# Performance work log

Measured on AMD Instinct MI355X. Metric: run time of the kernel, lower is better.

Reference implementation:

```python
import jax, jax.numpy as jnp
import numpy as np

K_NEIGHBOURS = 4  # neighbour_num
BN_EPS = 1e-5


def setup_inputs() -> dict:
    key = jax.random.key(0)
    ks = jax.random.split(key, 5)
    B, T, J, C = 32, 243, 17, 256
    std = np.sqrt(2.0 / C).astype(np.float32)
    return {
        "x": jax.random.normal(ks[0], (B, T, J, C), dtype=jnp.float32),
        "W_u": jax.random.normal(ks[1], (C, C), dtype=jnp.float32) * std,
        "b_u": jnp.zeros((C,), dtype=jnp.float32),
        "W_v": jax.random.normal(ks[2], (C, C), dtype=jnp.float32) * std,
        "b_v": jnp.zeros((C,), dtype=jnp.float32),
        "gamma": jnp.ones((T,), dtype=jnp.float32),
        "beta": jnp.zeros((T,), dtype=jnp.float32),
    }


def reference(x, W_u, b_u, W_v, b_v, gamma, beta):
    # temporal-mode GCN with top-k similarity adjacency
    b, t, j, c = x.shape
    xr = jnp.transpose(x, (0, 2, 1, 3)).reshape(b * j, t, c)  # [BJ, T, C]

    # similarity adjacency: keep edges >= k-th largest similarity per row
    sim = jnp.einsum('bnc,bmc->bnm', xr, xr)                  # [BJ, T, T]
    thr = jax.lax.top_k(sim, K_NEIGHBOURS)[0][..., -1:]       # [BJ, T, 1]
    adj = (sim >= thr).astype(x.dtype)

    # symmetric degree normalization D^{-1/2} A D^{-1/2}
    deg_inv_sqrt = adj.sum(-1) ** -0.5                        # [BJ, T]
    norm_adj = deg_inv_sqrt[:, :, None] * adj * deg_inv_sqrt[:, None, :]

    v = xr @ W_v.T + b_v
    u = xr @ W_u.T + b_u
    h = jnp.einsum('bnm,bmc->bnc', norm_adj, v) + u           # [BJ, T, C]

    # BatchNorm1d(num_features=T), training mode: stats over (batch, C)
    mean = h.mean(axis=(0, 2), keepdims=True)
    var = jnp.mean((h - mean) ** 2, axis=(0, 2), keepdims=True)
    hn = (h - mean) * jax.lax.rsqrt(var + BN_EPS) * gamma[None, :, None] + beta[None, :, None]

    out = jax.nn.relu(xr + hn)                                # residual (dim_in == dim_out)
    return jnp.transpose(out.reshape(b, j, t, c), (0, 2, 1, 3))  # [B, T, J, C]
```

## Files before the change

### kernel.cpp

```cpp
#include <hip/hip_runtime.h>

#define BB 32
#define TT 243
#define JJ 17
#define CC 256
#define BJC (BB*JJ)
#define MM (BJC*TT)
#define FR (BJC*256)
#define SIMP 244
#define NEG_INF (-3.0e38f)

typedef __attribute__((ext_vector_type(8))) short bf16x8;
typedef __attribute__((ext_vector_type(4))) float f32x4;
typedef __attribute__((ext_vector_type(8))) _Float16 f16x8;
typedef __attribute__((ext_vector_type(4))) _Float16 f16x4;

__device__ __forceinline__ unsigned short f2bf(float f) {
  unsigned int u = __float_as_uint(f);
  u = (u + 0x7fffu + ((u >> 16) & 1u)) >> 16;
  return (unsigned short)u;
}
__device__ __forceinline__ float bf2f(unsigned short s) {
  return __uint_as_float(((unsigned int)s) << 16);
}

__device__ __forceinline__ void gld16(const void* g, void* l) {
  __builtin_amdgcn_global_load_lds(
      (__attribute__((address_space(1))) void*)(g),
      (__attribute__((address_space(3))) void*)(l), 16, 0, 0);
}

__launch_bounds__(256)
__global__ void k_prep_w(const float* __restrict__ Wu, const float* __restrict__ Wv,
                         _Float16* __restrict__ wcp) {
  const int r = blockIdx.x * 4 + (threadIdx.x >> 6);
  const int l = threadIdx.x & 63;
  const float* src = ((r < CC) ? (Wu + (size_t)r * CC) : (Wv + (size_t)(r - CC) * CC)) + l * 4;
  float4 v = *reinterpret_cast<const float4*>(src);
  f16x4 hv = (f16x4){(_Float16)v.x, (_Float16)v.y, (_Float16)v.z, (_Float16)v.w};
  const int ks = l >> 4;
  const int u  = (l & 15) >> 1;
  const int s  = u ^ (r & 7);
  *reinterpret_cast<f16x4*>(wcp + ((size_t)ks * 512 + r) * 64 + s * 8 + (l & 1) * 4) = hv;
}

__launch_bounds__(256)
__global__ void k_prep_x(const float* __restrict__ x,
                         _Float16* __restrict__ xqh, _Float16* __restrict__ xql) {
  const int r = blockIdx.x * 4 + (threadIdx.x >> 6);
  const int l = threadIdx.x & 63;
  const int bj = r / TT, t = r - bj * TT;
  const int b = bj / JJ, j = bj - b * JJ;
  float4 v = *reinterpret_cast<const float4*>(
      x + ((size_t)(b * TT + t) * JJ + j) * CC + l * 4);
  _Float16 h0 = (_Float16)v.x, h1 = (_Float16)v.y, h2 = (_Float16)v.z, h3 = (_Float16)v.w;
  f16x4 hv = (f16x4){h0, h1, h2, h3};
  f16x4 lv = (f16x4){(_Float16)(v.x - (float)h0), (_Float16)(v.y - (float)h1),
                     (_Float16)(v.z - (float)h2), (_Float16)(v.w - (float)h3)};
  const int fr = bj * 256 + t;
  const int ks = l >> 4;
  const int u  = (l & 15) >> 1;
  const int s  = u ^ (t & 7);
  const size_t off = ((size_t)ks * FR + fr) * 64 + s * 8 + (l & 1) * 4;
  *reinterpret_cast<f16x4*>(xqh + off) = hv;
  *reinterpret_cast<f16x4*>(xql + off) = lv;
}

__launch_bounds__(512)
__global__ void k_sim(const _Float16* __restrict__ xqh, const _Float16* __restrict__ xql,
                      float* __restrict__ sim) {
  __shared__ _Float16 Sh[2][256 * 64];
  __shared__ _Float16 Sl[2][256 * 64];
  const int bj = blockIdx.x;
  const int tid = threadIdx.x, lane = tid & 63, wid = tid >> 6;
  const int wr = wid >> 2, wc = wid & 3;
  const int l15 = lane & 15, lg = lane >> 4;
  const size_t rb = (size_t)bj * 256;
  const size_t lsrc = (size_t)(lane >> 3) * 64 + (lane & 7) * 8;

  f32x4 acc[8][4];
  #pragma unroll
  for (int i = 0; i < 8; i++)
    #pragma unroll
    for (int j = 0; j < 4; j++) acc[i][j] = (f32x4){0.f, 0.f, 0.f, 0.f};

  auto STAGE = [&](int ks, int d) {
    const _Float16* ph = xqh + ((size_t)ks * FR + rb) * 64;
    const _Float16* pl = xql + ((size_t)ks * FR + rb) * 64;
    #pragma unroll
    for (int c = 0; c < 4; ++c) {
      const int row0 = (wid * 4 + c) * 8;
      gld16(ph + (size_t)row0 * 64 + lsrc, &Sh[d][row0 * 64]);
      gld16(pl + (size_t)row0 * 64 + lsrc, &Sl[d][row0 * 64]);
    }
  };
  auto COMPUTE = [&](int d) {
    #pragma unroll
    for (int kh = 0; kh < 2; ++kh) {
      f16x8 bhv[4], blv[4];
      #pragma unroll
      for (int j = 0; j < 4; ++j) {
        int rc = wc * 64 + j * 16 + l15;
        int sl = ((kh * 4 + lg) ^ (rc & 7)) * 8;
        bhv[j] = *reinterpret_cast<const f16x8*>(&Sh[d][rc * 64 + sl]);
        blv[j] = *reinterpret_cast<const f16x8*>(&Sl[d][rc * 64 + sl]);
      }
      #pragma unroll
      for (int i = 0; i < 8; ++i) {
        int rl = wr * 128 + i * 16 + l15;
        int sl = ((kh * 4 + lg) ^ (rl & 7)) * 8;
        f16x8 ah = *reinterpret_cast<const f16x8*>(&Sh[d][rl * 64 + sl]);
        f16x8 al = *reinterpret_cast<const f16x8*>(&Sl[d][rl * 64 + sl]);
        #pragma unroll
        for (int j = 0; j < 4; ++j) {
          acc[i][j] = __builtin_amdgcn_mfma_f32_16x16x32_f16(ah, bhv[j], acc[i][j], 0, 0, 0);
          acc[i][j] = __builtin_amdgcn_mfma_f32_16x16x32_f16(ah, blv[j], acc[i][j], 0, 0, 0);
          acc[i][j] = __builtin_amdgcn_mfma_f32_16x16x32_f16(al, bhv[j], acc[i][j], 0, 0, 0);
        }
      }
    }
  };

  STAGE(0, 0);
  __syncthreads();
  for (int ks = 0; ks < 4; ++ks) {
    if (ks < 3) STAGE(ks + 1, (ks + 1) & 1);
    COMPUTE(ks & 1);
    __syncthreads();
  }

  const size_t sbase = (size_t)bj * TT * SIMP;
  #pragma unroll
  for (int i = 0; i < 8; ++i) {
    #pragma unroll
    for (int q = 0; q < 4; ++q) {
      int n = wr * 128 + i * 16 + lg * 4 + q;
      if (n < TT) {
        #pragma unroll
        for (int j = 0; j < 4; ++j) {
          int c = wc * 64 + j * 16 + l15;
          if (c < TT) sim[sbase + (size_t)n * SIMP + c] = acc[i][j][q];
        }
      }
    }
  }
}

__launch_bounds__(256)
__global__ void k_uv(const _Float16* __restrict__ xqh, const _Float16* __restrict__ wcp,
                     const float* __restrict__ bu, const float* __restrict__ bv,
                     unsigned short* __restrict__ uo, unsigned short* __restrict__ vo) {
  __shared__ _Float16 S[2][128][64];
  const int ct = blockIdx.x;
  const int m0 = blockIdx.y * 128;
  const int tid = threadIdx.x, lane = tid & 63, wid = tid >> 6;
  const int rm = wid * 32;
  const int l15 = lane & 15, lg = lane >> 4;

  const float* bsrc = (ct < 2) ? bu : bv;
  unsigned short* osrc = (ct < 2) ? uo : vo;
  const int cb = (ct & 1) * 128;

  float bias[8];
  #pragma unroll
  for (int j = 0; j < 8; ++j) bias[j] = bsrc[cb + j * 16 + l15];

  f32x4 acc[2][8];
  #pragma unroll
  for (int i = 0; i < 2; i++)
    #pragma unroll
    for (int j = 0; j < 8; j++) acc[i][j] = (f32x4){0.f, 0.f, 0.f, 0.f};

  for (int ks = 0; ks < 4; ++ks) {
    #pragma unroll
    for (int c = 0; c < 8; ++c) {
      int ch = wid * 8 + c;
      int half = ch >> 4;
      int rows0 = (ch & 15) * 8;
      const _Float16* g = half
        ? wcp + ((size_t)ks * 512 + ct * 128 + rows0) * 64 + lane * 8
        : xqh + ((size_t)ks * FR  + m0       + rows0) * 64 + lane * 8;
      gld16(g, &S[half][rows0][0]);
    }
    __syncthreads();
    #pragma unroll
    for (int kh = 0; kh < 2; ++kh) {
      f16x8 af[2], bfv[8];
      #pragma unroll
      for (int i = 0; i < 2; ++i) {
        int rl = rm + i * 16 + l15;
        af[i] = *reinterpret_cast<const f16x8*>(&S[0][rl][((kh * 4 + lg) ^ (rl & 7)) * 8]);
      }
      #pragma unroll
      for (int j = 0; j < 8; ++j) {
        int rl = j * 16 + l15;
        bfv[j] = *reinterpret_cast<const f16x8*>(&S[1][rl][((kh * 4 + lg) ^ (rl & 7)) * 8]);
      }
      #pragma unroll
      for (int i = 0; i < 2; ++i)
        #pragma unroll
        for (int j = 0; j < 8; ++j)
          acc[i][j] = __builtin_amdgcn_mfma_f32_16x16x32_f16(af[i], bfv[j], acc[i][j], 0, 0, 0);
    }
    __syncthreads();
  }

  #pragma unroll
  for (int i = 0; i < 2; ++i) {
    #pragma unroll
    for (int q = 0; q < 4; ++q) {
      int gf = m0 + rm + i * 16 + lg * 4 + q;
      int t = gf & 255, bj = gf >> 8;
      if (t < TT) {
        size_t gm = (size_t)bj * TT + t;
        #pragma unroll
        for (int j = 0; j < 8; ++j)
          osrc[gm * CC + cb + j * 16 + l15] = f2bf(acc[i][j][q] + bias[j]);
      }
    }
  }
}

__launch_bounds__(256)
__global__ void k_topk(const float* __restrict__ sim,
                       float* __restrict__ dis_o,
                       unsigned long long* __restrict__ mask_o,
                       unsigned char* __restrict__ nbr_o,
                       unsigned char* __restrict__ deg_o) {
  const int l = threadIdx.x & 63, wv = threadIdx.x >> 6;
  const int r = blockIdx.x * 4 + wv;
  const float* row = sim + (size_t)r * SIMP;
  float o0 = (l       < TT) ? row[l]       : NEG_INF;
  float o1 = (l + 64  < TT) ? row[l + 64]  : NEG_INF;
  float o2 = (l + 128 < TT) ? row[l + 128] : NEG_INF;
  float o3 = (l + 192 < TT) ? row[l + 192] : NEG_INF;
  float v0 = o0, v1 = o1, v2 = o2, v3 = o3;
  { float mx, mn;
    mx=fmaxf(v0,v1); mn=fminf(v0,v1); v0=mx; v1=mn;
    mx=fmaxf(v2,v3); mn=fminf(v2,v3); v2=mx; v3=mn;
    mx=fmaxf(v0,v2); mn=fminf(v0,v2); v0=mx; v2=mn;
    mx=fmaxf(v1,v3); mn=fminf(v1,v3); v1=mx; v3=mn;
    mx=fmaxf(v1,v2); mn=fminf(v1,v2); v1=mx; v2=mn; }
  int p = 0;
  float thr = NEG_INF;
  #pragma unroll
  for (int it = 0; it < 4; ++it) {
    float head = (p == 0) ? v0 : (p == 1) ? v1 : (p == 2) ? v2 : (p == 3) ? v3 : NEG_INF;
    float m = head;
    #pragma unroll
    for (int off = 1; off < 64; off <<= 1) m = fmaxf(m, __shfl_xor(m, off));
    thr = m;
    unsigned long long msk = __ballot(head == m);
    int first = __ffsll(msk) - 1;
    if (l == first) p++;
  }
  unsigned long long m0 = __ballot(o0 >= thr);
  unsigned long long m1 = __ballot(o1 >= thr);
  unsigned long long m2 = __ballot(o2 >= thr);
  unsigned long long m3 = __ballot(o3 >= thr);
  const unsigned long long below = (1ull << l) - 1ull;
  const int b0 = __popcll(m0);
  const int b1 = b0 + __popcll(m1);
  const int b2 = b1 + __popcll(m2);
  const size_t r8 = (size_t)r * 8;
  if (o0 >= thr) { int q = __popcll(m0 & below);      if (q < 8) nbr_o[r8 + q] = (unsigned char)l; }
  if (o1 >= thr) { int q = b0 + __popcll(m1 & below); if (q < 8) nbr_o[r8 + q] = (unsigned char)(64 + l); }
  if (o2 >= thr) { int q = b1 + __popcll(m2 & below); if (q < 8) nbr_o[r8 + q] = (unsigned char)(128 + l); }
  if (o3 >= thr) { int q = b2 + __popcll(m3 & below); if (q < 8) nbr_o[r8 + q] = (unsigned char)(192 + l); }
  if (l == 0) {
    int deg = b2 + __popcll(m3);
    dis_o[r] = rsqrtf((float)deg);
    deg_o[r] = (unsigned char)((deg > 255) ? 255 : deg);
    mask_o[(size_t)r * 4 + 0] = m0;
    mask_o[(size_t)r * 4 + 1] = m1;
    mask_o[(size_t)r * 4 + 2] = m2;
    mask_o[(size_t)r * 4 + 3] = m3;
  }
}

__launch_bounds__(512)
__global__ void k_agg(const unsigned char* __restrict__ nbr,
                      const unsigned char* __restrict__ degv,
                      const unsigned long long* __restrict__ mask,
                      const float* __restrict__ dis,
                      const unsigned short* __restrict__ u,
                      const unsigned short* __restrict__ v,
                      unsigned short* __restrict__ h,
                      float* __restrict__ p1, float* __restrict__ p2) {
  __shared__ float dis_l[256];
  const int bj = blockIdx.x;
  const int tid = threadIdx.x, lane = tid & 63, wid = tid >> 6;
  if (tid < TT) dis_l[tid] = dis[(size_t)bj * TT + tid];
  __syncthreads();
  const int start = blockIdx.y * 122;
  const int cnt = blockIdx.y ? (TT - 122) : 122;
  const size_t pbase = (size_t)bj * TT;
  const int co = lane * 4;
  for (int rl = wid; rl < cnt; rl += 8) {
    const int t = start + rl;
    const size_t r = pbase + t;
    const float dr = dis_l[t];
    const int dg = degv[r];
    const unsigned long long nb = *reinterpret_cast<const unsigned long long*>(nbr + r * 8);
    ushort4 uu = *reinterpret_cast<const ushort4*>(u + r * CC + co);
    float a0 = bf2f(uu.x), a1 = bf2f(uu.y), a2 = bf2f(uu.z), a3 = bf2f(uu.w);
    if (dg <= 8) {
      const int i0 = (int)(nb & 255), i1 = (int)((nb >> 8) & 255),
                i2 = (int)((nb >> 16) & 255), i3 = (int)((nb >> 24) & 255);
      ushort4 w0v = *reinterpret_cast<const ushort4*>(v + (pbase + i0) * CC + co);
      ushort4 w1v = *reinterpret_cast<const ushort4*>(v + (pbase + i1) * CC + co);
      ushort4 w2v = *reinterpret_cast<const ushort4*>(v + (pbase + i2) * CC + co);
      ushort4 w3v = *reinterpret_cast<const ushort4*>(v + (pbase + i3) * CC + co);
      const float w0 = dr * dis_l[i0], w1 = dr * dis_l[i1],
                  w2 = dr * dis_l[i2], w3 = dr * dis_l[i3];
      a0 = __builtin_fmaf(w0, bf2f(w0v.x), a0); a1 = __builtin_fmaf(w0, bf2f(w0v.y), a1);
      a2 = __builtin_fmaf(w0, bf2f(w0v.z), a2); a3 = __builtin_fmaf(w0, bf2f(w0v.w), a3);
      a0 = __builtin_fmaf(w1, bf2f(w1v.x), a0); a1 = __builtin_fmaf(w1, bf2f(w1v.y), a1);
      a2 = __builtin_fmaf(w1, bf2f(w1v.z), a2); a3 = __builtin_fmaf(w1, bf2f(w1v.w), a3);
      a0 = __builtin_fmaf(w2, bf2f(w2v.x), a0); a1 = __builtin_fmaf(w2, bf2f(w2v.y), a1);
      a2 = __builtin_fmaf(w2, bf2f(w2v.z), a2); a3 = __builtin_fmaf(w2, bf2f(w2v.w), a3);
      a0 = __builtin_fmaf(w3, bf2f(w3v.x), a0); a1 = __builtin_fmaf(w3, bf2f(w3v.y), a1);
      a2 = __builtin_fmaf(w3, bf2f(w3v.z), a2); a3 = __builtin_fmaf(w3, bf2f(w3v.w), a3);
      #pragma unroll
      for (int e = 4; e < 8; ++e) {
        if (e < dg) {
          const int ix = (int)((nb >> (8 * e)) & 255);
          const float we = dr * dis_l[ix];
          ushort4 vv = *reinterpret_cast<const ushort4*>(v + (pbase + ix) * CC + co);
          a0 = __builtin_fmaf(we, bf2f(vv.x), a0); a1 = __builtin_fmaf(we, bf2f(vv.y), a1);
          a2 = __builtin_fmaf(we, bf2f(vv.z), a2); a3 = __builtin_fmaf(we, bf2f(vv.w), a3);
        }
      }
    } else {
      #pragma unroll
      for (int w4 = 0; w4 < 4; ++w4) {
        unsigned long long m = mask[r * 4 + w4];
        while (m) {
          int i = __ffsll(m) - 1;
          m &= m - 1;
          int idx = w4 * 64 + i;
          float w = dr * dis_l[idx];
          ushort4 vv = *reinterpret_cast<const ushort4*>(v + (pbase + idx) * CC + co);
          a0 = __builtin_fmaf(w, bf2f(vv.x), a0);
          a1 = __builtin_fmaf(w, bf2f(vv.y), a1);
          a2 = __builtin_fmaf(w, bf2f(vv.z), a2);
          a3 = __builtin_fmaf(w, bf2f(vv.w), a3);
        }
      }
    }
    ushort4 hh;
    hh.x = f2bf(a0); hh.y = f2bf(a1); hh.z = f2bf(a2); hh.w = f2bf(a3);
    *reinterpret_cast<ushort4*>(h + r * CC + co) = hh;
    float s1 = a0 + a1 + a2 + a3;
    float s2 = a0*a0 + a1*a1 + a2*a2 + a3*a3;
    #pragma unroll
    for (int off = 1; off < 64; off <<= 1) { s1 += __shfl_xor(s1, off); s2 += __shfl_xor(s2, off); }
    if (lane == 0) { p1[r] = s1; p2[r] = s2; }
  }
}

__global__ void k_bnstat(const float* __restrict__ p1, const float* __restrict__ p2,
                         const float* __restrict__ gamma, const float* __restrict__ beta,
                         float* __restrict__ scale, float* __restrict__ shift) {
  __shared__ float sA[256], sB[256];
  const int t = blockIdx.x;
  const int tid = threadIdx.x;
  float a = 0.f, b2 = 0.f;
  for (int bj = tid; bj < BJC; bj += 256) {
    a  += p1[bj * TT + t];
    b2 += p2[bj * TT + t];
  }
  sA[tid] = a; sB[tid] = b2;
  __syncthreads();
  for (int s = 128; s > 0; s >>= 1) {
    if (tid < s) { sA[tid] += sA[tid + s]; sB[tid] += sB[tid + s]; }
    __syncthreads();
  }
  if (tid == 0) {
    const float invN = 1.0f / (float)(BJC * CC);
    float mean = sA[0] * invN;
    float var  = sB[0] * invN - mean * mean;
    float sc   = rsqrtf(var + 1e-5f) * gamma[t];
    scale[t] = sc;
    shift[t] = beta[t] - mean * sc;
  }
}

__global__ void k_out(const float* __restrict__ x, const unsigned short* __restrict__ h,
                      const float* __restrict__ scale, const float* __restrict__ shift,
                      float* __restrict__ out) {
  int g = blockIdx.x * 256 + threadIdx.x;
  if (g >= MM * (CC/4)) return;
  int c4  = g & 63;
  int rowx = g >> 6;
  int b   = rowx / (TT*JJ);
  int rem = rowx - b*(TT*JJ);
  int t   = rem / JJ;
  int j   = rem - t*JJ;
  size_t hoff = ((size_t)(b*JJ + j) * TT + t) * CC + c4*4;
  float4 xv = *reinterpret_cast<const float4*>(x + (size_t)rowx*CC + c4*4);
  ushort4 hv = *reinterpret_cast<const ushort4*>(h + hoff);
  float sc = scale[t], sh = shift[t];
  float4 o;
  o.x = fmaxf(xv.x + bf2f(hv.x)*sc + sh, 0.f);
  o.y = fmaxf(xv.y + bf2f(hv.y)*sc + sh, 0.f);
  o.z = fmaxf(xv.z + bf2f(hv.z)*sc + sh, 0.f);
  o.w = fmaxf(xv.w + bf2f(hv.w)*sc + sh, 0.f);
  *reinterpret_cast<float4*>(out + (size_t)rowx*CC + c4*4) = o;
}

extern "C" void kernel_launch(void* const* d_in, const int* in_sizes, int n_in,
                              void* d_out, int out_size, void* d_ws, size_t ws_size,
                              hipStream_t stream) {
  const float* x     = (const float*)d_in[0];
  const float* Wu    = (const float*)d_in[1];
  const float* bu    = (const float*)d_in[2];
  const float* Wv    = (const float*)d_in[3];
  const float* bv    = (const float*)d_in[4];
  const float* gamma = (const float*)d_in[5];
  const float* beta  = (const float*)d_in[6];
  float* out = (float*)d_out;

  char* ws = (char*)d_ws;
  size_t off = 0;
  auto alloc = [&](size_t bytes) -> void* {
    void* p = ws + off;
    off = (off + bytes + 255) & ~(size_t)255;
    return p;
  };
  _Float16* xqh = (_Float16*)alloc((size_t)4 * FR * 64 * 2);
  _Float16* xql = (_Float16*)alloc((size_t)4 * FR * 64 * 2);
  _Float16* wcp = (_Float16*)alloc((size_t)4 * 512 * 64 * 2);
  float* sim = (float*)alloc((size_t)BJC * TT * SIMP * 4);
  float* dis = (float*)alloc((size_t)MM * 4);
  unsigned long long* msk = (unsigned long long*)alloc((size_t)MM * 4 * 8);
  unsigned char* nbr = (unsigned char*)alloc((size_t)MM * 8);
  unsigned char* deg = (unsigned char*)alloc((size_t)MM);
  float* p1    = (float*)alloc((size_t)MM * 4);
  float* p2    = (float*)alloc((size_t)MM * 4);
  float* scale = (float*)alloc(1024);
  float* shift = (float*)alloc(1024);
  unsigned short* v = (unsigned short*)alloc((size_t)MM * CC * 2);
  unsigned short* u = (unsigned short*)sim;
  unsigned short* h = (unsigned short*)xql;

  if (ws_size < off) {
    hipMemsetAsync(d_out, 0, (size_t)out_size * 4, stream);
    return;
  }

  k_prep_w<<<dim3(512/4), dim3(256), 0, stream>>>(Wu, Wv, wcp);
  k_prep_x<<<dim3(MM/4), dim3(256), 0, stream>>>(x, xqh, xql);
  k_sim  <<<dim3(BJC), dim3(512), 0, stream>>>(xqh, xql, sim);
  k_topk <<<dim3(MM/4), dim3(256), 0, stream>>>(sim, dis, msk, nbr, deg);
  k_uv   <<<dim3(4, FR/128), dim3(256), 0, stream>>>(xqh, wcp, bu, bv, u, v);
  k_agg  <<<dim3(BJC, 2), dim3(512), 0, stream>>>(nbr, deg, msk, dis, u, v, h, p1, p2);
  k_bnstat<<<dim3(TT), dim3(256), 0, stream>>>(p1, p2, gamma, beta, scale, shift);
  k_out  <<<dim3((MM*(CC/4) + 255)/256), dim3(256), 0, stream>>>(x, h, scale, shift, out);
}
```

Baseline: 384.4 us.

## Fuse top-k selection into similarity kernel via LDS staging

```diff
diff --git a/kernel.cpp b/kernel.cpp
--- a/kernel.cpp
+++ b/kernel.cpp
@@ -7,8 +7,8 @@
 #define BJC (BB*JJ)
 #define MM (BJC*TT)
 #define FR (BJC*256)
-#define SIMP 244
 #define NEG_INF (-3.0e38f)
+#define SST 244
 
 typedef __attribute__((ext_vector_type(8))) short bf16x8;
 typedef __attribute__((ext_vector_type(4))) float f32x4;
@@ -68,9 +68,11 @@
 
 __launch_bounds__(512)
 __global__ void k_sim(const _Float16* __restrict__ xqh, const _Float16* __restrict__ xql,
-                      float* __restrict__ sim) {
-  __shared__ _Float16 Sh[2][256 * 64];
-  __shared__ _Float16 Sl[2][256 * 64];
+                      float* __restrict__ dis_o,
+                      unsigned long long* __restrict__ mask_o,
+                      unsigned char* __restrict__ nbr_o,
+                      unsigned char* __restrict__ deg_o) {
+  __shared__ __align__(16) char LRAW[131072];
   const int bj = blockIdx.x;
   const int tid = threadIdx.x, lane = tid & 63, wid = tid >> 6;
   const int wr = wid >> 2, wc = wid & 3;
@@ -84,17 +86,22 @@
     #pragma unroll
     for (int j = 0; j < 4; j++) acc[i][j] = (f32x4){0.f, 0.f, 0.f, 0.f};
 
+  auto SH = [&](int d) -> _Float16* { return (_Float16*)(LRAW + d * 32768); };
+  auto SL = [&](int d) -> _Float16* { return (_Float16*)(LRAW + 65536 + d * 32768); };
+
   auto STAGE = [&](int ks, int d) {
     const _Float16* ph = xqh + ((size_t)ks * FR + rb) * 64;
     const _Float16* pl = xql + ((size_t)ks * FR + rb) * 64;
     #pragma unroll
     for (int c = 0; c < 4; ++c) {
       const int row0 = (wid * 4 + c) * 8;
-      gld16(ph + (size_t)row0 * 64 + lsrc, &Sh[d][row0 * 64]);
-      gld16(pl + (size_t)row0 * 64 + lsrc, &Sl[d][row0 * 64]);
+      gld16(ph + (size_t)row0 * 64 + lsrc, SH(d) + row0 * 64);
+      gld16(pl + (size_t)row0 * 64 + lsrc, SL(d) + row0 * 64);
     }
   };
   auto COMPUTE = [&](int d) {
+    const _Float16* sh = SH(d);
+    const _Float16* sl_ = SL(d);
     #pragma unroll
     for (int kh = 0; kh < 2; ++kh) {
       f16x8 bhv[4], blv[4];
@@ -102,15 +109,15 @@
       for (int j = 0; j < 4; ++j) {
         int rc = wc * 64 + j * 16 + l15;
         int sl = ((kh * 4 + lg) ^ (rc & 7)) * 8;
-        bhv[j] = *reinterpret_cast<const f16x8*>(&Sh[d][rc * 64 + sl]);
-        blv[j] = *reinterpret_cast<const f16x8*>(&Sl[d][rc * 64 + sl]);
+        bhv[j] = *reinterpret_cast<const f16x8*>(&sh[rc * 64 + sl]);
+        blv[j] = *reinterpret_cast<const f16x8*>(&sl_[rc * 64 + sl]);
       }
       #pragma unroll
       for (int i = 0; i < 8; ++i) {
         int rl = wr * 128 + i * 16 + l15;
         int sl = ((kh * 4 + lg) ^ (rl & 7)) * 8;
-        f16x8 ah = *reinterpret_cast<const f16x8*>(&Sh[d][rl * 64 + sl]);
-        f16x8 al = *reinterpret_cast<const f16x8*>(&Sl[d][rl * 64 + sl]);
+        f16x8 ah = *reinterpret_cast<const f16x8*>(&sh[rl * 64 + sl]);
+        f16x8 al = *reinterpret_cast<const f16x8*>(&sl_[rl * 64 + sl]);
         #pragma unroll
         for (int j = 0; j < 4; ++j) {
           acc[i][j] = __builtin_amdgcn_mfma_f32_16x16x32_f16(ah, bhv[j], acc[i][j], 0, 0, 0);
@@ -129,20 +136,78 @@
     __syncthreads();
   }
 
-  const size_t sbase = (size_t)bj * TT * SIMP;
-  #pragma unroll
-  for (int i = 0; i < 8; ++i) {
-    #pragma unroll
-    for (int q = 0; q < 4; ++q) {
-      int n = wr * 128 + i * 16 + lg * 4 + q;
-      if (n < TT) {
+  float* simt = (float*)LRAW;
+  #pragma unroll 1
+  for (int half = 0; half < 2; ++half) {
+    if (wr == half) {
+      #pragma unroll
+      for (int i = 0; i < 8; ++i) {
         #pragma unroll
-        for (int j = 0; j < 4; ++j) {
-          int c = wc * 64 + j * 16 + l15;
-          if (c < TT) sim[sbase + (size_t)n * SIMP + c] = acc[i][j][q];
+        for (int q = 0; q < 4; ++q) {
+          int rloc = i * 16 + lg * 4 + q;
+          if (half * 128 + rloc < TT) {
+            #pragma unroll
+            for (int j = 0; j < 4; ++j) {
+              int c = wc * 64 + j * 16 + l15;
+              if (c < SST) simt[rloc * SST + c] = acc[i][j][q];
+            }
+          }
         }
       }
     }
+    __syncthreads();
+    const int nrows = half ? (TT - 128) : 128;
+    for (int rloc = wid; rloc < nrows; rloc += 8) {
+      const float* row = &simt[rloc * SST];
+      float o0 = row[lane];
+      float o1 = row[lane + 64];
+      float o2 = row[lane + 128];
+      float o3 = (lane + 192 < TT) ? row[lane + 192] : NEG_INF;
+      float v0 = o0, v1 = o1, v2 = o2, v3 = o3;
+      { float mx, mn;
+        mx=fmaxf(v0,v1); mn=fminf(v0,v1); v0=mx; v1=mn;
+        mx=fmaxf(v2,v3); mn=fminf(v2,v3); v2=mx; v3=mn;
+        mx=fmaxf(v0,v2); mn=fminf(v0,v2); v0=mx; v2=mn;
+        mx=fmaxf(v1,v3); mn=fminf(v1,v3); v1=mx; v3=mn;
+        mx=fmaxf(v1,v2); mn=fminf(v1,v2); v1=mx; v2=mn; }
+      int p = 0;
+      float thr = NEG_INF;
+      #pragma unroll
+      for (int it = 0; it < 4; ++it) {
+        float head = (p == 0) ? v0 : (p == 1) ? v1 : (p == 2) ? v2 : (p == 3) ? v3 : NEG_INF;
+        float m = head;
+        #pragma unroll
+        for (int off = 1; off < 64; off <<= 1) m = fmaxf(m, __shfl_xor(m, off));
+        thr = m;
+        unsigned long long msk = __ballot(head == m);
+        int first = __ffsll(msk) - 1;
+        if (lane == first) p++;
+      }
+      unsigned long long m0 = __ballot(o0 >= thr);
+      unsigned long long m1 = __ballot(o1 >= thr);
+      unsigned long long m2 = __ballot(o2 >= thr);
+      unsigned long long m3 = __ballot(o3 >= thr);
+      const unsigned long long below = (1ull << lane) - 1ull;
+      const int b0 = __popcll(m0);
+      const int b1 = b0 + __popcll(m1);
+      const int b2 = b1 + __popcll(m2);
+      const size_t r = (size_t)bj * TT + half * 128 + rloc;
+      const size_t r8 = r * 8;
+      if (o0 >= thr) { int q = __popcll(m0 & below);      if (q < 8) nbr_o[r8 + q] = (unsigned char)lane; }
+      if (o1 >= thr) { int q = b0 + __popcll(m1 & below); if (q < 8) nbr_o[r8 + q] = (unsigned char)(64 + lane); }
+      if (o2 >= thr) { int q = b1 + __popcll(m2 & below); if (q < 8) nbr_o[r8 + q] = (unsigned char)(128 + lane); }
+      if (o3 >= thr) { int q = b2 + __popcll(m3 & below); if (q < 8) nbr_o[r8 + q] = (unsigned char)(192 + lane); }
+      if (lane == 0) {
+        int deg = b2 + __popcll(m3);
+        dis_o[r] = rsqrtf((float)deg);
+        deg_o[r] = (unsigned char)((deg > 255) ? 255 : deg);
+        mask_o[r * 4 + 0] = m0;
+        mask_o[r * 4 + 1] = m1;
+        mask_o[r * 4 + 2] = m2;
+        mask_o[r * 4 + 3] = m3;
+      }
+    }
+    __syncthreads();
   }
 }
 
@@ -218,63 +283,6 @@
           osrc[gm * CC + cb + j * 16 + l15] = f2bf(acc[i][j][q] + bias[j]);
       }
     }
-  }
-}
-
-__launch_bounds__(256)
-__global__ void k_topk(const float* __restrict__ sim,
-                       float* __restrict__ dis_o,
-                       unsigned long long* __restrict__ mask_o,
-                       unsigned char* __restrict__ nbr_o,
-                       unsigned char* __restrict__ deg_o) {
-  const int l = threadIdx.x & 63, wv = threadIdx.x >> 6;
-  const int r = blockIdx.x * 4 + wv;
-  const float* row = sim + (size_t)r * SIMP;
-  float o0 = (l       < TT) ? row[l]       : NEG_INF;
-  float o1 = (l + 64  < TT) ? row[l + 64]  : NEG_INF;
-  float o2 = (l + 128 < TT) ? row[l + 128] : NEG_INF;
-  float o3 = (l + 192 < TT) ? row[l + 192] : NEG_INF;
-  float v0 = o0, v1 = o1, v2 = o2, v3 = o3;
-  { float mx, mn;
-    mx=fmaxf(v0,v1); mn=fminf(v0,v1); v0=mx; v1=mn;
-    mx=fmaxf(v2,v3); mn=fminf(v2,v3); v2=mx; v3=mn;
-    mx=fmaxf(v0,v2); mn=fminf(v0,v2); v0=mx; v2=mn;
-    mx=fmaxf(v1,v3); mn=fminf(v1,v3); v1=mx; v3=mn;
-    mx=fmaxf(v1,v2); mn=fminf(v1,v2); v1=mx; v2=mn; }
-  int p = 0;
-  float thr = NEG_INF;
-  #pragma unroll
-  for (int it = 0; it < 4; ++it) {
-    float head = (p == 0) ? v0 : (p == 1) ? v1 : (p == 2) ? v2 : (p == 3) ? v3 : NEG_INF;
-    float m = head;
-    #pragma unroll
-    for (int off = 1; off < 64; off <<= 1) m = fmaxf(m, __shfl_xor(m, off));
-    thr = m;
-    unsigned long long msk = __ballot(head == m);
-    int first = __ffsll(msk) - 1;
-    if (l == first) p++;
-  }
-  unsigned long long m0 = __ballot(o0 >= thr);
-  unsigned long long m1 = __ballot(o1 >= thr);
-  unsigned long long m2 = __ballot(o2 >= thr);
-  unsigned long long m3 = __ballot(o3 >= thr);
-  const unsigned long long below = (1ull << l) - 1ull;
-  const int b0 = __popcll(m0);
-  const int b1 = b0 + __popcll(m1);
-  const int b2 = b1 + __popcll(m2);
-  const size_t r8 = (size_t)r * 8;
-  if (o0 >= thr) { int q = __popcll(m0 & below);      if (q < 8) nbr_o[r8 + q] = (unsigned char)l; }
-  if (o1 >= thr) { int q = b0 + __popcll(m1 & below); if (q < 8) nbr_o[r8 + q] = (unsigned char)(64 + l); }
-  if (o2 >= thr) { int q = b1 + __popcll(m2 & below); if (q < 8) nbr_o[r8 + q] = (unsigned char)(128 + l); }
-  if (o3 >= thr) { int q = b2 + __popcll(m3 & below); if (q < 8) nbr_o[r8 + q] = (unsigned char)(192 + l); }
-  if (l == 0) {
-    int deg = b2 + __popcll(m3);
-    dis_o[r] = rsqrtf((float)deg);
-    deg_o[r] = (unsigned char)((deg > 255) ? 255 : deg);
-    mask_o[(size_t)r * 4 + 0] = m0;
-    mask_o[(size_t)r * 4 + 1] = m1;
-    mask_o[(size_t)r * 4 + 2] = m2;
-    mask_o[(size_t)r * 4 + 3] = m3;
   }
 }
 
@@ -431,7 +439,6 @@
   _Float16* xqh = (_Float16*)alloc((size_t)4 * FR * 64 * 2);
   _Float16* xql = (_Float16*)alloc((size_t)4 * FR * 64 * 2);
   _Float16* wcp = (_Float16*)alloc((size_t)4 * 512 * 64 * 2);
-  float* sim = (float*)alloc((size_t)BJC * TT * SIMP * 4);
   float* dis = (float*)alloc((size_t)MM * 4);
   unsigned long long* msk = (unsigned long long*)alloc((size_t)MM * 4 * 8);
   unsigned char* nbr = (unsigned char*)alloc((size_t)MM * 8);
@@ -440,8 +447,8 @@
   float* p2    = (float*)alloc((size_t)MM * 4);
   float* scale = (float*)alloc(1024);
   float* shift = (float*)alloc(1024);
+  unsigned short* u = (unsigned short*)alloc((size_t)MM * CC * 2);
   unsigned short* v = (unsigned short*)alloc((size_t)MM * CC * 2);
-  unsigned short* u = (unsigned short*)sim;
   unsigned short* h = (unsigned short*)xql;
 
   if (ws_size < off) {
@@ -451,8 +458,7 @@
 
   k_prep_w<<<dim3(512/4), dim3(256), 0, stream>>>(Wu, Wv, wcp);
   k_prep_x<<<dim3(MM/4), dim3(256), 0, stream>>>(x, xqh, xql);
-  k_sim  <<<dim3(BJC), dim3(512), 0, stream>>>(xqh, xql, sim);
-  k_topk <<<dim3(MM/4), dim3(256), 0, stream>>>(sim, dis, msk, nbr, deg);
+  k_sim  <<<dim3(BJC), dim3(512), 0, stream>>>(xqh, xql, dis, msk, nbr, deg);
   k_uv   <<<dim3(4, FR/128), dim3(256), 0, stream>>>(xqh, wcp, bu, bv, u, v);
   k_agg  <<<dim3(BJC, 2), dim3(512), 0, stream>>>(nbr, deg, msk, dis, u, v, h, p1, p2);
   k_bnstat<<<dim3(TT), dim3(256), 0, stream>>>(p1, p2, gamma, beta, scale, shift);
```

New measurement: 435.3 us. 13.3% more time.

## Single-buffer sim LDS staging and use bitonic-merge butterfly for top-4 threshold

Applied to the files above, without the earlier changes.

```diff
diff --git a/kernel.cpp b/kernel.cpp
--- a/kernel.cpp
+++ b/kernel.cpp
@@ -69,8 +69,8 @@
 __launch_bounds__(512)
 __global__ void k_sim(const _Float16* __restrict__ xqh, const _Float16* __restrict__ xql,
                       float* __restrict__ sim) {
-  __shared__ _Float16 Sh[2][256 * 64];
-  __shared__ _Float16 Sl[2][256 * 64];
+  __shared__ _Float16 Sh[256 * 64];
+  __shared__ _Float16 Sl[256 * 64];
   const int bj = blockIdx.x;
   const int tid = threadIdx.x, lane = tid & 63, wid = tid >> 6;
   const int wr = wid >> 2, wc = wid & 3;
@@ -84,17 +84,18 @@
     #pragma unroll
     for (int j = 0; j < 4; j++) acc[i][j] = (f32x4){0.f, 0.f, 0.f, 0.f};
 
-  auto STAGE = [&](int ks, int d) {
-    const _Float16* ph = xqh + ((size_t)ks * FR + rb) * 64;
-    const _Float16* pl = xql + ((size_t)ks * FR + rb) * 64;
-    #pragma unroll
-    for (int c = 0; c < 4; ++c) {
-      const int row0 = (wid * 4 + c) * 8;
-      gld16(ph + (size_t)row0 * 64 + lsrc, &Sh[d][row0 * 64]);
-      gld16(pl + (size_t)row0 * 64 + lsrc, &Sl[d][row0 * 64]);
-    }
-  };
-  auto COMPUTE = [&](int d) {
+  for (int ks = 0; ks < 4; ++ks) {
+    {
+      const _Float16* ph = xqh + ((size_t)ks * FR + rb) * 64;
+      const _Float16* pl = xql + ((size_t)ks * FR + rb) * 64;
+      #pragma unroll
+      for (int c = 0; c < 4; ++c) {
+        const int row0 = (wid * 4 + c) * 8;
+        gld16(ph + (size_t)row0 * 64 + lsrc, &Sh[row0 * 64]);
+        gld16(pl + (size_t)row0 * 64 + lsrc, &Sl[row0 * 64]);
+      }
+    }
+    __syncthreads();
     #pragma unroll
     for (int kh = 0; kh < 2; ++kh) {
       f16x8 bhv[4], blv[4];
@@ -102,15 +103,15 @@
       for (int j = 0; j < 4; ++j) {
         int rc = wc * 64 + j * 16 + l15;
         int sl = ((kh * 4 + lg) ^ (rc & 7)) * 8;
-        bhv[j] = *reinterpret_cast<const f16x8*>(&Sh[d][rc * 64 + sl]);
-        blv[j] = *reinterpret_cast<const f16x8*>(&Sl[d][rc * 64 + sl]);
+        bhv[j] = *reinterpret_cast<const f16x8*>(&Sh[rc * 64 + sl]);
+        blv[j] = *reinterpret_cast<const f16x8*>(&Sl[rc * 64 + sl]);
       }
       #pragma unroll
       for (int i = 0; i < 8; ++i) {
         int rl = wr * 128 + i * 16 + l15;
         int sl = ((kh * 4 + lg) ^ (rl & 7)) * 8;
-        f16x8 ah = *reinterpret_cast<const f16x8*>(&Sh[d][rl * 64 + sl]);
-        f16x8 al = *reinterpret_cast<const f16x8*>(&Sl[d][rl * 64 + sl]);
+        f16x8 ah = *reinterpret_cast<const f16x8*>(&Sh[rl * 64 + sl]);
+        f16x8 al = *reinterpret_cast<const f16x8*>(&Sl[rl * 64 + sl]);
         #pragma unroll
         for (int j = 0; j < 4; ++j) {
           acc[i][j] = __builtin_amdgcn_mfma_f32_16x16x32_f16(ah, bhv[j], acc[i][j], 0, 0, 0);
@@ -119,14 +120,7 @@
         }
       }
     }
-  };
-
-  STAGE(0, 0);
-  __syncthreads();
-  for (int ks = 0; ks < 4; ++ks) {
-    if (ks < 3) STAGE(ks + 1, (ks + 1) & 1);
-    COMPUTE(ks & 1);
-    __syncthreads();
+    if (ks < 3) __syncthreads();
   }
 
   const size_t sbase = (size_t)bj * TT * SIMP;
@@ -230,9 +224,9 @@
   const int l = threadIdx.x & 63, wv = threadIdx.x >> 6;
   const int r = blockIdx.x * 4 + wv;
   const float* row = sim + (size_t)r * SIMP;
-  float o0 = (l       < TT) ? row[l]       : NEG_INF;
-  float o1 = (l + 64  < TT) ? row[l + 64]  : NEG_INF;
-  float o2 = (l + 128 < TT) ? row[l + 128] : NEG_INF;
+  float o0 = row[l];
+  float o1 = row[l + 64];
+  float o2 = row[l + 128];
   float o3 = (l + 192 < TT) ? row[l + 192] : NEG_INF;
   float v0 = o0, v1 = o1, v2 = o2, v3 = o3;
   { float mx, mn;
@@ -241,19 +235,21 @@
     mx=fmaxf(v0,v2); mn=fminf(v0,v2); v0=mx; v2=mn;
     mx=fmaxf(v1,v3); mn=fminf(v1,v3); v1=mx; v3=mn;
     mx=fmaxf(v1,v2); mn=fminf(v1,v2); v1=mx; v2=mn; }
-  int p = 0;
-  float thr = NEG_INF;
-  #pragma unroll
-  for (int it = 0; it < 4; ++it) {
-    float head = (p == 0) ? v0 : (p == 1) ? v1 : (p == 2) ? v2 : (p == 3) ? v3 : NEG_INF;
-    float m = head;
-    #pragma unroll
-    for (int off = 1; off < 64; off <<= 1) m = fmaxf(m, __shfl_xor(m, off));
-    thr = m;
-    unsigned long long msk = __ballot(head == m);
-    int first = __ffsll(msk) - 1;
-    if (l == first) p++;
-  }
+  #pragma unroll
+  for (int off = 1; off < 64; off <<= 1) {
+    float b0 = __shfl_xor(v0, off), b1 = __shfl_xor(v1, off),
+          b2 = __shfl_xor(v2, off), b3 = __shfl_xor(v3, off);
+    float t0 = fmaxf(v0, b3), t1 = fmaxf(v1, b2),
+          t2 = fmaxf(v2, b1), t3 = fmaxf(v3, b0);
+    float mx, mn;
+    mx=fmaxf(t0,t2); mn=fminf(t0,t2); t0=mx; t2=mn;
+    mx=fmaxf(t1,t3); mn=fminf(t1,t3); t1=mx; t3=mn;
+    mx=fmaxf(t0,t1); mn=fminf(t0,t1); t0=mx; t1=mn;
+    mx=fmaxf(t2,t3); mn=fminf(t2,t3); t2=mx; t3=mn;
+    v0=t0; v1=t1; v2=t2; v3=t3;
+  }
+  const float thr = v3;
+
   unsigned long long m0 = __ballot(o0 >= thr);
   unsigned long long m1 = __ballot(o1 >= thr);
   unsigned long long m2 = __ballot(o2 >= thr);
```

After: 387.0 us. About the same (+0.7%).
